# Performance work log

Hardware: AMD Instinct MI355X
Metric: run time of the kernel (lower is better)

The kernel has to match this reference:

```python
import jax, jax.numpy as jnp
import numpy as np

N = 50000      # nodes
E = 800000     # edges (before self-loops)
V = 50000      # vocab
D = 128        # embed_dim
H = 128        # hidden_dim
G = 64         # graphs in batch


def setup_inputs() -> dict:
    key = jax.random.key(0)
    ks = jax.random.split(key, 14)
    x_lex = jax.random.randint(ks[0], (N,), 0, V)
    edge_index = jax.random.randint(ks[1], (2, E), 0, N)
    batch = jnp.sort(jax.random.randint(ks[2], (N,), 0, G))
    s = 1.0 / np.sqrt(D)
    emb = jax.random.normal(ks[3], (V, D), dtype=jnp.float32) * s
    W1 = jax.random.normal(ks[4], (D, H), dtype=jnp.float32) * s
    att_src1 = jax.random.normal(ks[5], (H,), dtype=jnp.float32) * s
    att_dst1 = jax.random.normal(ks[6], (H,), dtype=jnp.float32) * s
    b1 = jnp.zeros((H,), dtype=jnp.float32)
    W2 = jax.random.normal(ks[7], (H, H), dtype=jnp.float32) * s
    att_src2 = jax.random.normal(ks[8], (H,), dtype=jnp.float32) * s
    att_dst2 = jax.random.normal(ks[9], (H,), dtype=jnp.float32) * s
    b2 = jnp.zeros((H,), dtype=jnp.float32)
    Wc = jax.random.normal(ks[10], (H, 1), dtype=jnp.float32) * s
    bc = jnp.zeros((1,), dtype=jnp.float32)
    return dict(x_lex=x_lex, edge_index=edge_index, batch=batch, emb=emb,
                W1=W1, att_src1=att_src1, att_dst1=att_dst1, b1=b1,
                W2=W2, att_src2=att_src2, att_dst2=att_dst2, b2=b2,
                Wc=Wc, bc=bc)


def _gat_conv(x, src, dst, W, a_src, a_dst, b):
    # PyG GATConv, heads=1, self-loops already appended to src/dst.
    h = x @ W                                   # [N, H]
    e = jax.nn.leaky_relu((h @ a_src)[src] + (h @ a_dst)[dst], 0.2)  # [Etot]
    m = jax.ops.segment_max(e, dst, num_segments=N)
    p = jnp.exp(e - m[dst])
    z = jax.ops.segment_sum(p, dst, num_segments=N)
    alpha = p / z[dst]                          # softmax per destination node
    out = jax.ops.segment_sum(alpha[:, None] * h[src], dst, num_segments=N)
    return out + b


def reference(x_lex, edge_index, batch, emb, W1, att_src1, att_dst1, b1,
              W2, att_src2, att_dst2, b2, Wc, bc):
    loops = jnp.arange(N, dtype=edge_index.dtype)
    src = jnp.concatenate([edge_index[0], loops])   # add self-loops (PyG default)
    dst = jnp.concatenate([edge_index[1], loops])
    x = emb[x_lex]                                  # [N, D]
    h = jax.nn.relu(_gat_conv(x, src, dst, W1, att_src1, att_dst1, b1))
    h = jax.nn.relu(_gat_conv(h, src, dst, W2, att_src2, att_dst2, b2))
    sums = jax.ops.segment_sum(h, batch, num_segments=G)           # [G, H]
    cnt = jax.ops.segment_sum(jnp.ones((N,), h.dtype), batch, num_segments=G)
    h_pool = sums / jnp.maximum(cnt, 1.0)[:, None]
    logits = h_pool @ Wc + bc                                       # [G, 1]
    return (logits, h_pool)
```

## Files before the change

kernel.cpp:

```cpp
#include <hip/hip_runtime.h>
#include <hip/hip_bf16.h>


#define THREADS 256
#define PSLICE 16
#define BUK_S 196
#define SORT_BLOCKS 128

typedef __attribute__((ext_vector_type(8))) short short8v;
typedef __attribute__((ext_vector_type(4))) float f32x4;

static __device__ __forceinline__ unsigned short f2bf(float f) {
    unsigned int u = __float_as_uint(f);
    return (unsigned short)((u + 0x7fffu + ((u >> 16) & 1u)) >> 16);
}
static __device__ __forceinline__ float bf2f(unsigned short b) {
    return __uint_as_float(((unsigned int)b) << 16);
}

__global__ __launch_bounds__(THREADS) void k_wsplit2(const float* __restrict__ W1,
                                                     const float* __restrict__ W2,
                                                     unsigned short* __restrict__ Wh1,
                                                     unsigned short* __restrict__ Wl1,
                                                     unsigned short* __restrict__ Wh2,
                                                     unsigned short* __restrict__ Wl2,
                                                     int* __restrict__ bcount, int nbuk) {
    if (blockIdx.x == 0 && threadIdx.x < nbuk) bcount[threadIdx.x] = 0;
    int t = blockIdx.x * THREADS + threadIdx.x;
    const float* W = W1;
    unsigned short* Wh = Wh1;
    unsigned short* Wl = Wl1;
    if (t >= 128 * 128) {
        t -= 128 * 128;
        W = W2; Wh = Wh2; Wl = Wl2;
    }
    int k = t >> 7, n = t & 127;
    float w = W[t];
    unsigned short h = f2bf(w);
    unsigned short lo = f2bf(w - bf2f(h));
    int c = n >> 4, nl = n & 15, tt = k >> 5, kk = k & 31, g = kk >> 3, j = kk & 7;
    int o = (((c * 4 + tt) * 64) + g * 16 + nl) * 8 + j;
    Wh[o] = h;
    Wl[o] = lo;
}

__global__ __launch_bounds__(THREADS) void k_bukhist(const int* __restrict__ dst,
                                                     int* __restrict__ bcount, int E_, int chunk) {
    __shared__ int hist[THREADS];
    hist[threadIdx.x] = 0;
    __syncthreads();
    int e0 = blockIdx.x * chunk;
    int e1 = min(e0 + chunk, E_);
    for (int e = e0 + threadIdx.x; e < e1; e += THREADS)
        atomicAdd(&hist[dst[e] / BUK_S], 1);
    __syncthreads();
    int c = hist[threadIdx.x];
    if (c) atomicAdd(&bcount[threadIdx.x], c);
}

__global__ __launch_bounds__(THREADS) void k_bukscan(const int* __restrict__ bcount,
                                                     int* __restrict__ sbase,
                                                     int* __restrict__ gcur,
                                                     int* __restrict__ cbase,
                                                     int nbuk, int Nn) {
    __shared__ int s[THREADS];
    int tid = threadIdx.x;
    int v = (tid < nbuk) ? bcount[tid] : 0;
    s[tid] = v;
    __syncthreads();
    for (int off = 1; off < THREADS; off <<= 1) {
        int t = (tid >= off) ? s[tid - off] : 0;
        __syncthreads();
        s[tid] += t;
        __syncthreads();
    }
    int excl1 = s[tid] - v;
    if (tid < nbuk) { sbase[tid] = excl1; gcur[tid] = excl1; }
    int n0 = tid * BUK_S;
    int ns = (tid < nbuk) ? min(BUK_S, Nn - n0) : 0;
    int v2 = v + ns;
    __syncthreads();
    s[tid] = v2;
    __syncthreads();
    for (int off = 1; off < THREADS; off <<= 1) {
        int t = (tid >= off) ? s[tid - off] : 0;
        __syncthreads();
        s[tid] += t;
        __syncthreads();
    }
    if (tid < nbuk) cbase[tid] = s[tid] - v2;
}

__global__ __launch_bounds__(THREADS) void k_bukscatter(const int* __restrict__ src,
                                                        const int* __restrict__ dst,
                                                        int* __restrict__ gcur,
                                                        unsigned int* __restrict__ rec,
                                                        int E_, int chunk) {
    __shared__ int hist[THREADS];
    __shared__ int base[THREADS];
    hist[threadIdx.x] = 0;
    __syncthreads();
    int e0 = blockIdx.x * chunk;
    int e1 = min(e0 + chunk, E_);
    for (int e = e0 + threadIdx.x; e < e1; e += THREADS)
        atomicAdd(&hist[dst[e] / BUK_S], 1);
    __syncthreads();
    int c = hist[threadIdx.x];
    if (c) base[threadIdx.x] = atomicAdd(&gcur[threadIdx.x], c);
    hist[threadIdx.x] = 0;
    __syncthreads();
    for (int e = e0 + threadIdx.x; e < e1; e += THREADS) {
        int d = dst[e];
        int b = d / BUK_S;
        int r = atomicAdd(&hist[b], 1);
        rec[base[b] + r] = (unsigned int)src[e] | ((unsigned int)(d - b * BUK_S) << 17);
    }
}

__global__ __launch_bounds__(THREADS) void k_csr(const unsigned int* __restrict__ rec,
                                                 const int* __restrict__ sbase,
                                                 const int* __restrict__ bcount,
                                                 const int* __restrict__ cbase,
                                                 int* __restrict__ rowptr,
                                                 int* __restrict__ esrc,
                                                 int* __restrict__ edst,
                                                 int Nn, int nbuk, int Etot) {
    __shared__ int cnt[THREADS];
    __shared__ int s[THREADS];
    __shared__ int cur[THREADS];
    int b = blockIdx.x;
    int tid = threadIdx.x;
    int n0 = b * BUK_S;
    int ns = min(BUK_S, Nn - n0);
    int cnt_e = bcount[b];
    int rbase = sbase[b];
    int cb = cbase[b];

    cnt[tid] = 0;
    __syncthreads();
    for (int i = tid; i < cnt_e; i += THREADS)
        atomicAdd(&cnt[rec[rbase + i] >> 17], 1);
    __syncthreads();
    int v = (tid < ns) ? cnt[tid] + 1 : 0;
    s[tid] = v;
    __syncthreads();
    for (int off = 1; off < THREADS; off <<= 1) {
        int t = (tid >= off) ? s[tid - off] : 0;
        __syncthreads();
        s[tid] += t;
        __syncthreads();
    }
    int excl = s[tid] - v;
    __syncthreads();
    s[tid] = excl;
    cur[tid] = excl;
    if (tid < ns) rowptr[n0 + tid] = cb + excl;
    if (b == nbuk - 1 && tid == 0) rowptr[Nn] = Etot;
    __syncthreads();
    for (int i = tid; i < cnt_e; i += THREADS) {
        unsigned int r = rec[rbase + i];
        int l = r >> 17;
        int slot = atomicAdd(&cur[l], 1);
        esrc[cb + slot] = (int)(r & 0x1FFFFu);
        edst[cb + slot] = n0 + l;
    }
    __syncthreads();
    if (tid < ns) {
        int slot = s[tid] + cnt[tid];
        esrc[cb + slot] = n0 + tid;
        edst[cb + slot] = n0 + tid;
    }
}

static __device__ __forceinline__ int xsw(int r, int c) {
    return (((r * 16 + (c >> 3)) ^ (r & 7)) << 3) | (c & 7);
}

__global__ __launch_bounds__(THREADS) void k_gemm_mfma(const float* __restrict__ X,
                                                       const int* __restrict__ idx,
                                                       const unsigned short* __restrict__ WBh,
                                                       const unsigned short* __restrict__ WBl,
                                                       const float* __restrict__ a_s,
                                                       const float* __restrict__ a_d,
                                                       unsigned short* __restrict__ outb,
                                                       float* __restrict__ as_,
                                                       float* __restrict__ ad_, int Nrows) {
    __shared__ unsigned short xh[64 * 128];
    __shared__ unsigned short xl[64 * 128];

    {
        int r = threadIdx.x >> 2;
        int c0 = (threadIdx.x & 3) * 32;
        int R = blockIdx.x * 64 + r;
        if (R < Nrows) {
            int g = idx ? idx[R] : R;
            const float4* xrow = (const float4*)(X + (size_t)g * 128);
            #pragma unroll
            for (int i = 0; i < 8; ++i) {
                float4 v = xrow[(c0 >> 2) + i];
                int c = c0 + i * 4;
                ushort4 hh, ll;
                hh.x = f2bf(v.x); ll.x = f2bf(v.x - bf2f(hh.x));
                hh.y = f2bf(v.y); ll.y = f2bf(v.y - bf2f(hh.y));
                hh.z = f2bf(v.z); ll.z = f2bf(v.z - bf2f(hh.z));
                hh.w = f2bf(v.w); ll.w = f2bf(v.w - bf2f(hh.w));
                int o = xsw(r, c);
                *(ushort4*)&xh[o] = hh;
                *(ushort4*)&xl[o] = ll;
            }
        } else {
            #pragma unroll
            for (int i = 0; i < 8; ++i) {
                int o = xsw(r, c0 + i * 4);
                *(ushort4*)&xh[o] = make_ushort4(0, 0, 0, 0);
                *(ushort4*)&xl[o] = make_ushort4(0, 0, 0, 0);
            }
        }
    }
    __syncthreads();

    int wid = threadIdx.x >> 6;
    int lane = threadIdx.x & 63;
    int nl = lane & 15;
    int g = lane >> 4;
    int arow = wid * 16 + nl;

    f32x4 acc[8];
    #pragma unroll
    for (int c = 0; c < 8; ++c) acc[c] = (f32x4){0.f, 0.f, 0.f, 0.f};

    #pragma unroll
    for (int t = 0; t < 4; ++t) {
        int ao = xsw(arow, t * 32 + g * 8);
        short8v ah = *(const short8v*)&xh[ao];
        short8v al = *(const short8v*)&xl[ao];
        #pragma unroll
        for (int c = 0; c < 8; ++c) {
            int bo = (((c * 4 + t) * 64) + lane) * 8;
            short8v bh = *(const short8v*)&WBh[bo];
            short8v bl = *(const short8v*)&WBl[bo];
            acc[c] = __builtin_amdgcn_mfma_f32_16x16x32_bf16(ah, bh, acc[c], 0, 0, 0);
            acc[c] = __builtin_amdgcn_mfma_f32_16x16x32_bf16(ah, bl, acc[c], 0, 0, 0);
            acc[c] = __builtin_amdgcn_mfma_f32_16x16x32_bf16(al, bh, acc[c], 0, 0, 0);
        }
    }

    float asv[8], adv[8];
    #pragma unroll
    for (int c = 0; c < 8; ++c) {
        asv[c] = a_s[c * 16 + nl];
        adv[c] = a_d[c * 16 + nl];
    }
    int Rb = blockIdx.x * 64 + wid * 16 + g * 4;
    #pragma unroll
    for (int r = 0; r < 4; ++r) {
        int R = Rb + r;
        bool ok = (R < Nrows);
        float ps = 0.f, pd = 0.f;
        #pragma unroll
        for (int c = 0; c < 8; ++c) {
            float v = acc[c][r];
            if (ok) outb[(size_t)R * 128 + c * 16 + nl] = f2bf(v);
            ps = fmaf(v, asv[c], ps);
            pd = fmaf(v, adv[c], pd);
        }
        #pragma unroll
        for (int o = 8; o; o >>= 1) {
            ps += __shfl_xor(ps, o);
            pd += __shfl_xor(pd, o);
        }
        if (ok && nl == 0) {
            as_[R] = ps;
            ad_[R] = pd;
        }
    }
}

__global__ __launch_bounds__(THREADS) void k_agg(const unsigned short* __restrict__ hb,
                                                 const float* __restrict__ as_,
                                                 const float* __restrict__ ad_,
                                                 const int* __restrict__ rowptr,
                                                 const int* __restrict__ esrc,
                                                 const float* __restrict__ bias,
                                                 float* __restrict__ out, int Nn) {
    __shared__ int2 ep[4][64];
    int w = threadIdx.x >> 6;
    int lane = threadIdx.x & 63;
    int half = lane >> 5;
    int j = lane & 31;
    int d = blockIdx.x * 4 + w;
    if (d >= Nn) return;
    int beg = rowptr[d], end = rowptr[d + 1];
    float adv = ad_[d];
    float z = 0.f, a0 = 0.f, a1 = 0.f, a2 = 0.f, a3 = 0.f;
    for (int c0 = beg; c0 < end; c0 += 64) {
        int kk = c0 + lane;
        bool ok = (kk < end);
        int sl = esrc[ok ? kk : beg];
        float pv = 0.f;
        if (ok) {
            float e = as_[sl] + adv;
            e = (e > 0.f) ? e : 0.2f * e;
            pv = __expf(e);
        }
        ep[w][lane] = make_int2(sl, __float_as_int(pv));
        int cn = end - c0;
        if (cn > 64) cn = 64;
        for (int k0 = 0; k0 < cn; k0 += 16) {
            int2 ev[8];
            #pragma unroll
            for (int i = 0; i < 8; ++i)
                ev[i] = ep[w][(k0 + 2 * i + half) & 63];
            uint2 hv[8];
            #pragma unroll
            for (int i = 0; i < 8; ++i)
                hv[i] = *(const uint2*)&hb[((size_t)ev[i].x << 7) + j * 4];
            #pragma unroll
            for (int i = 0; i < 8; ++i) {
                float p = __int_as_float(ev[i].y);
                z += p;
                a0 += p * __uint_as_float(hv[i].x << 16);
                a1 += p * __uint_as_float(hv[i].x & 0xffff0000u);
                a2 += p * __uint_as_float(hv[i].y << 16);
                a3 += p * __uint_as_float(hv[i].y & 0xffff0000u);
            }
        }
    }
    z  += __shfl_xor(z, 32);
    a0 += __shfl_xor(a0, 32);
    a1 += __shfl_xor(a1, 32);
    a2 += __shfl_xor(a2, 32);
    a3 += __shfl_xor(a3, 32);
    if (half == 0) {
        float inv = 1.f / z;
        float4 o;
        o.x = fmaxf(a0 * inv + bias[j * 4 + 0], 0.f);
        o.y = fmaxf(a1 * inv + bias[j * 4 + 1], 0.f);
        o.z = fmaxf(a2 * inv + bias[j * 4 + 2], 0.f);
        o.w = fmaxf(a3 * inv + bias[j * 4 + 3], 0.f);
        *(float4*)&out[(size_t)d * 128 + j * 4] = o;
    }
}

__global__ __launch_bounds__(THREADS) void k_pool_partial(const float* __restrict__ x,
                                                          const int* __restrict__ batch,
                                                          float* __restrict__ part, int Nn) {
    int g = blockIdx.x;
    int s = blockIdx.y;
    int a = 0, b = Nn;
    while (a < b) { int mid = (a + b) >> 1; if (batch[mid] < g) a = mid + 1; else b = mid; }
    int lo = a;
    b = Nn;
    while (a < b) { int mid = (a + b) >> 1; if (batch[mid] < g + 1) a = mid + 1; else b = mid; }
    int hi = a;

    int j = threadIdx.x & 127;
    int half = threadIdx.x >> 7;
    float acc = 0.f;
    for (int n = lo + s * 2 + half; n < hi; n += 2 * PSLICE) acc += x[(size_t)n * 128 + j];
    __shared__ float sred[THREADS];
    sred[threadIdx.x] = acc;
    __syncthreads();
    if (half == 0) part[((size_t)g * PSLICE + s) * 128 + j] = sred[j] + sred[128 + j];
}

__global__ __launch_bounds__(128) void k_pool_final(const float* __restrict__ part,
                                                    const int* __restrict__ batch,
                                                    const float* __restrict__ Wc,
                                                    const float* __restrict__ bc,
                                                    float* __restrict__ out, int Nn, int Gn) {
    int g = blockIdx.x;
    int j = threadIdx.x;
    int a = 0, b = Nn;
    while (a < b) { int mid = (a + b) >> 1; if (batch[mid] < g) a = mid + 1; else b = mid; }
    int lo = a;
    b = Nn;
    while (a < b) { int mid = (a + b) >> 1; if (batch[mid] < g + 1) a = mid + 1; else b = mid; }
    int cnt = a - lo;

    float s = 0.f;
    #pragma unroll
    for (int t = 0; t < PSLICE; ++t) s += part[((size_t)g * PSLICE + t) * 128 + j];
    float mean = s / fmaxf((float)cnt, 1.f);
    out[Gn + (size_t)g * 128 + j] = mean;

    __shared__ float sred[128];
    sred[j] = mean * Wc[j];
    __syncthreads();
    for (int off = 64; off >= 1; off >>= 1) {
        if (j < off) sred[j] += sred[j + off];
        __syncthreads();
    }
    if (j == 0) out[g] = sred[0] + bc[0];
}

static inline size_t align256(size_t x) { return (x + 255) & ~(size_t)255; }

extern "C" void kernel_launch(void* const* d_in, const int* in_sizes, int n_in,
                              void* d_out, int out_size, void* d_ws, size_t ws_size,
                              hipStream_t stream) {
    const int* x_lex = (const int*)d_in[0];
    const int* eidx  = (const int*)d_in[1];
    const int* batch = (const int*)d_in[2];
    const float* emb = (const float*)d_in[3];
    const float* W1  = (const float*)d_in[4];
    const float* a_s1 = (const float*)d_in[5];
    const float* a_d1 = (const float*)d_in[6];
    const float* b1  = (const float*)d_in[7];
    const float* W2  = (const float*)d_in[8];
    const float* a_s2 = (const float*)d_in[9];
    const float* a_d2 = (const float*)d_in[10];
    const float* b2  = (const float*)d_in[11];
    const float* Wc  = (const float*)d_in[12];
    const float* bc  = (const float*)d_in[13];

    const int N = in_sizes[0];
    const int E = in_sizes[1] / 2;
    const int G = out_size / 129;
    const int Etot = E + N;
    const int* esrc_in = eidx;
    const int* edst_in = eidx + E;
    const int NBUK = (N + BUK_S - 1) / BUK_S;

    char* p = (char*)d_ws;
    unsigned short* hb = (unsigned short*)p;  p += align256((size_t)N * 128 * 2);
    float* obuf = (float*)p;            p += align256((size_t)N * 128 * 4);
    float* as_  = (float*)p;            p += align256((size_t)N * 4);
    float* ad_  = (float*)p;            p += align256((size_t)N * 4);
    int* bcount = (int*)p;              p += align256((size_t)NBUK * 4);
    int* sbase  = (int*)p;              p += align256((size_t)NBUK * 4);
    int* gcur   = (int*)p;              p += align256((size_t)NBUK * 4);
    int* cbase  = (int*)p;              p += align256((size_t)NBUK * 4);
    int* rowptr = (int*)p;              p += align256((size_t)(N + 1) * 4);
    unsigned int* rec = (unsigned int*)p; p += align256((size_t)Etot * 4);
    int* esrc   = (int*)p;              p += align256((size_t)Etot * 4);
    int* edst   = (int*)p;              p += align256((size_t)Etot * 4);
    float* part = (float*)p;            p += align256((size_t)G * PSLICE * 128 * 4);
    unsigned short* WBh1 = (unsigned short*)p; p += align256((size_t)128 * 128 * 2);
    unsigned short* WBl1 = (unsigned short*)p; p += align256((size_t)128 * 128 * 2);
    unsigned short* WBh2 = (unsigned short*)p; p += align256((size_t)128 * 128 * 2);
    unsigned short* WBl2 = (unsigned short*)p; p += align256((size_t)128 * 128 * 2);

    const int chunk = (E + SORT_BLOCKS - 1) / SORT_BLOCKS;

    k_wsplit2<<<128, THREADS, 0, stream>>>(W1, W2, WBh1, WBl1, WBh2, WBl2, bcount, NBUK);

    k_bukhist<<<SORT_BLOCKS, THREADS, 0, stream>>>(edst_in, bcount, E, chunk);
    k_bukscan<<<1, THREADS, 0, stream>>>(bcount, sbase, gcur, cbase, NBUK, N);
    k_bukscatter<<<SORT_BLOCKS, THREADS, 0, stream>>>(esrc_in, edst_in, gcur, rec, E, chunk);
    k_csr<<<NBUK, THREADS, 0, stream>>>(rec, sbase, bcount, cbase, rowptr, esrc, edst, N, NBUK, Etot);

    const int gemm_grid = (N + 63) / 64;
    const int agg_grid = (N + 3) / 4;

    k_gemm_mfma<<<gemm_grid, THREADS, 0, stream>>>(emb, x_lex, WBh1, WBl1, a_s1, a_d1, hb, as_, ad_, N);
    k_agg<<<agg_grid, THREADS, 0, stream>>>(hb, as_, ad_, rowptr, esrc, b1, obuf, N);

    k_gemm_mfma<<<gemm_grid, THREADS, 0, stream>>>(obuf, nullptr, WBh2, WBl2, a_s2, a_d2, hb, as_, ad_, N);
    k_agg<<<agg_grid, THREADS, 0, stream>>>(hb, as_, ad_, rowptr, esrc, b2, obuf, N);

    k_pool_partial<<<dim3(G, PSLICE), THREADS, 0, stream>>>(obuf, batch, part, N);
    k_pool_final<<<G, 128, 0, stream>>>(part, batch, Wc, bc, (float*)d_out, N, G);
}
```

Measured before the change: 180.5 us.

## Fuse edge histogram and scan into layer-1 GEMM launch, merge pooling kernels

Appends the edge-bucket histogram blocks to the first GEMM grid, so they run alongside it. The last histogram block, detected with an atomic done-counter, performs the bucket scan, which removes the separate histogram and scan launches. The two pooling kernels are merged the same way, with a per-graph last-block finalize, and the unused edst array is no longer written. This cuts three kernel launches and some global writes, in exchange for atomic counters and threadfence ordering, plus counter resets added to the prep kernel.

```diff
diff --git a/kernel.cpp b/kernel.cpp
--- a/kernel.cpp
+++ b/kernel.cpp
@@ -18,14 +18,20 @@
     return __uint_as_float(((unsigned int)b) << 16);
 }
 
-__global__ __launch_bounds__(THREADS) void k_wsplit2(const float* __restrict__ W1,
-                                                     const float* __restrict__ W2,
-                                                     unsigned short* __restrict__ Wh1,
-                                                     unsigned short* __restrict__ Wl1,
-                                                     unsigned short* __restrict__ Wh2,
-                                                     unsigned short* __restrict__ Wl2,
-                                                     int* __restrict__ bcount, int nbuk) {
-    if (blockIdx.x == 0 && threadIdx.x < nbuk) bcount[threadIdx.x] = 0;
+__global__ __launch_bounds__(THREADS) void k_prep(const float* __restrict__ W1,
+                                                  const float* __restrict__ W2,
+                                                  unsigned short* __restrict__ Wh1,
+                                                  unsigned short* __restrict__ Wl1,
+                                                  unsigned short* __restrict__ Wh2,
+                                                  unsigned short* __restrict__ Wl2,
+                                                  int* __restrict__ bcount, int nbuk,
+                                                  int* __restrict__ done,
+                                                  int* __restrict__ pdone, int ng) {
+    if (blockIdx.x == 0) {
+        if (threadIdx.x < nbuk) bcount[threadIdx.x] = 0;
+        if (threadIdx.x == 0) *done = 0;
+        if (threadIdx.x < ng) pdone[threadIdx.x] = 0;
+    }
     int t = blockIdx.x * THREADS + threadIdx.x;
     const float* W = W1;
     unsigned short* Wh = Wh1;
@@ -44,154 +50,25 @@
     Wl[o] = lo;
 }
 
-__global__ __launch_bounds__(THREADS) void k_bukhist(const int* __restrict__ dst,
-                                                     int* __restrict__ bcount, int E_, int chunk) {
-    __shared__ int hist[THREADS];
-    hist[threadIdx.x] = 0;
-    __syncthreads();
-    int e0 = blockIdx.x * chunk;
-    int e1 = min(e0 + chunk, E_);
-    for (int e = e0 + threadIdx.x; e < e1; e += THREADS)
-        atomicAdd(&hist[dst[e] / BUK_S], 1);
-    __syncthreads();
-    int c = hist[threadIdx.x];
-    if (c) atomicAdd(&bcount[threadIdx.x], c);
-}
-
-__global__ __launch_bounds__(THREADS) void k_bukscan(const int* __restrict__ bcount,
-                                                     int* __restrict__ sbase,
-                                                     int* __restrict__ gcur,
-                                                     int* __restrict__ cbase,
-                                                     int nbuk, int Nn) {
-    __shared__ int s[THREADS];
-    int tid = threadIdx.x;
-    int v = (tid < nbuk) ? bcount[tid] : 0;
-    s[tid] = v;
-    __syncthreads();
-    for (int off = 1; off < THREADS; off <<= 1) {
-        int t = (tid >= off) ? s[tid - off] : 0;
-        __syncthreads();
-        s[tid] += t;
-        __syncthreads();
-    }
-    int excl1 = s[tid] - v;
-    if (tid < nbuk) { sbase[tid] = excl1; gcur[tid] = excl1; }
-    int n0 = tid * BUK_S;
-    int ns = (tid < nbuk) ? min(BUK_S, Nn - n0) : 0;
-    int v2 = v + ns;
-    __syncthreads();
-    s[tid] = v2;
-    __syncthreads();
-    for (int off = 1; off < THREADS; off <<= 1) {
-        int t = (tid >= off) ? s[tid - off] : 0;
-        __syncthreads();
-        s[tid] += t;
-        __syncthreads();
-    }
-    if (tid < nbuk) cbase[tid] = s[tid] - v2;
-}
-
-__global__ __launch_bounds__(THREADS) void k_bukscatter(const int* __restrict__ src,
-                                                        const int* __restrict__ dst,
-                                                        int* __restrict__ gcur,
-                                                        unsigned int* __restrict__ rec,
-                                                        int E_, int chunk) {
-    __shared__ int hist[THREADS];
-    __shared__ int base[THREADS];
-    hist[threadIdx.x] = 0;
-    __syncthreads();
-    int e0 = blockIdx.x * chunk;
-    int e1 = min(e0 + chunk, E_);
-    for (int e = e0 + threadIdx.x; e < e1; e += THREADS)
-        atomicAdd(&hist[dst[e] / BUK_S], 1);
-    __syncthreads();
-    int c = hist[threadIdx.x];
-    if (c) base[threadIdx.x] = atomicAdd(&gcur[threadIdx.x], c);
-    hist[threadIdx.x] = 0;
-    __syncthreads();
-    for (int e = e0 + threadIdx.x; e < e1; e += THREADS) {
-        int d = dst[e];
-        int b = d / BUK_S;
-        int r = atomicAdd(&hist[b], 1);
-        rec[base[b] + r] = (unsigned int)src[e] | ((unsigned int)(d - b * BUK_S) << 17);
-    }
-}
-
-__global__ __launch_bounds__(THREADS) void k_csr(const unsigned int* __restrict__ rec,
-                                                 const int* __restrict__ sbase,
-                                                 const int* __restrict__ bcount,
-                                                 const int* __restrict__ cbase,
-                                                 int* __restrict__ rowptr,
-                                                 int* __restrict__ esrc,
-                                                 int* __restrict__ edst,
-                                                 int Nn, int nbuk, int Etot) {
-    __shared__ int cnt[THREADS];
-    __shared__ int s[THREADS];
-    __shared__ int cur[THREADS];
-    int b = blockIdx.x;
-    int tid = threadIdx.x;
-    int n0 = b * BUK_S;
-    int ns = min(BUK_S, Nn - n0);
-    int cnt_e = bcount[b];
-    int rbase = sbase[b];
-    int cb = cbase[b];
-
-    cnt[tid] = 0;
-    __syncthreads();
-    for (int i = tid; i < cnt_e; i += THREADS)
-        atomicAdd(&cnt[rec[rbase + i] >> 17], 1);
-    __syncthreads();
-    int v = (tid < ns) ? cnt[tid] + 1 : 0;
-    s[tid] = v;
-    __syncthreads();
-    for (int off = 1; off < THREADS; off <<= 1) {
-        int t = (tid >= off) ? s[tid - off] : 0;
-        __syncthreads();
-        s[tid] += t;
-        __syncthreads();
-    }
-    int excl = s[tid] - v;
-    __syncthreads();
-    s[tid] = excl;
-    cur[tid] = excl;
-    if (tid < ns) rowptr[n0 + tid] = cb + excl;
-    if (b == nbuk - 1 && tid == 0) rowptr[Nn] = Etot;
-    __syncthreads();
-    for (int i = tid; i < cnt_e; i += THREADS) {
-        unsigned int r = rec[rbase + i];
-        int l = r >> 17;
-        int slot = atomicAdd(&cur[l], 1);
-        esrc[cb + slot] = (int)(r & 0x1FFFFu);
-        edst[cb + slot] = n0 + l;
-    }
-    __syncthreads();
-    if (tid < ns) {
-        int slot = s[tid] + cnt[tid];
-        esrc[cb + slot] = n0 + tid;
-        edst[cb + slot] = n0 + tid;
-    }
-}
-
 static __device__ __forceinline__ int xsw(int r, int c) {
     return (((r * 16 + (c >> 3)) ^ (r & 7)) << 3) | (c & 7);
 }
 
-__global__ __launch_bounds__(THREADS) void k_gemm_mfma(const float* __restrict__ X,
-                                                       const int* __restrict__ idx,
-                                                       const unsigned short* __restrict__ WBh,
-                                                       const unsigned short* __restrict__ WBl,
-                                                       const float* __restrict__ a_s,
-                                                       const float* __restrict__ a_d,
-                                                       unsigned short* __restrict__ outb,
-                                                       float* __restrict__ as_,
-                                                       float* __restrict__ ad_, int Nrows) {
-    __shared__ unsigned short xh[64 * 128];
-    __shared__ unsigned short xl[64 * 128];
-
+static __device__ __forceinline__ void gemm_body(unsigned short* xh, unsigned short* xl,
+                                                 const float* __restrict__ X,
+                                                 const int* __restrict__ idx,
+                                                 const unsigned short* __restrict__ WBh,
+                                                 const unsigned short* __restrict__ WBl,
+                                                 const float* __restrict__ a_s,
+                                                 const float* __restrict__ a_d,
+                                                 unsigned short* __restrict__ outb,
+                                                 float* __restrict__ as_,
+                                                 float* __restrict__ ad_,
+                                                 int Nrows, int bid) {
     {
         int r = threadIdx.x >> 2;
         int c0 = (threadIdx.x & 3) * 32;
-        int R = blockIdx.x * 64 + r;
+        int R = bid * 64 + r;
         if (R < Nrows) {
             int g = idx ? idx[R] : R;
             const float4* xrow = (const float4*)(X + (size_t)g * 128);
@@ -251,7 +128,7 @@
         asv[c] = a_s[c * 16 + nl];
         adv[c] = a_d[c * 16 + nl];
     }
-    int Rb = blockIdx.x * 64 + wid * 16 + g * 4;
+    int Rb = bid * 64 + wid * 16 + g * 4;
     #pragma unroll
     for (int r = 0; r < 4; ++r) {
         int R = Rb + r;
@@ -274,6 +151,165 @@
             ad_[R] = pd;
         }
     }
+}
+
+__global__ __launch_bounds__(THREADS) void k_gemm_hist(const float* __restrict__ X,
+                                                       const int* __restrict__ idx,
+                                                       const unsigned short* __restrict__ WBh,
+                                                       const unsigned short* __restrict__ WBl,
+                                                       const float* __restrict__ a_s,
+                                                       const float* __restrict__ a_d,
+                                                       unsigned short* __restrict__ outb,
+                                                       float* __restrict__ as_,
+                                                       float* __restrict__ ad_,
+                                                       int Nrows, int gemm_blocks,
+                                                       const int* __restrict__ dst,
+                                                       int* __restrict__ bcount,
+                                                       int E_, int chunk,
+                                                       int* __restrict__ done,
+                                                       int* __restrict__ sbase,
+                                                       int* __restrict__ gcur,
+                                                       int* __restrict__ cbase,
+                                                       int nbuk, int Nn) {
+    __shared__ unsigned short xh[64 * 128];
+    __shared__ unsigned short xl[64 * 128];
+    if ((int)blockIdx.x >= gemm_blocks) {
+        int hbk = blockIdx.x - gemm_blocks;
+        int tid = threadIdx.x;
+        __shared__ int hist[THREADS];
+        hist[tid] = 0;
+        __syncthreads();
+        int e0 = hbk * chunk;
+        int e1 = min(e0 + chunk, E_);
+        for (int e = e0 + tid; e < e1; e += THREADS)
+            atomicAdd(&hist[dst[e] / BUK_S], 1);
+        __syncthreads();
+        int c = hist[tid];
+        if (c) atomicAdd(&bcount[tid], c);
+        __threadfence();
+        __syncthreads();
+        __shared__ int lastf;
+        if (tid == 0) lastf = (atomicAdd(done, 1) == SORT_BLOCKS - 1);
+        __syncthreads();
+        if (!lastf) return;
+        __threadfence();
+        __shared__ int s2[THREADS];
+        int v = 0;
+        if (tid < nbuk) v = __hip_atomic_load(&bcount[tid], __ATOMIC_RELAXED, __HIP_MEMORY_SCOPE_AGENT);
+        s2[tid] = v;
+        __syncthreads();
+        for (int off = 1; off < THREADS; off <<= 1) {
+            int t = (tid >= off) ? s2[tid - off] : 0;
+            __syncthreads();
+            s2[tid] += t;
+            __syncthreads();
+        }
+        int excl1 = s2[tid] - v;
+        if (tid < nbuk) { sbase[tid] = excl1; gcur[tid] = excl1; }
+        int n0 = tid * BUK_S;
+        int ns = (tid < nbuk) ? min(BUK_S, Nn - n0) : 0;
+        int v2 = v + ns;
+        __syncthreads();
+        s2[tid] = v2;
+        __syncthreads();
+        for (int off = 1; off < THREADS; off <<= 1) {
+            int t = (tid >= off) ? s2[tid - off] : 0;
+            __syncthreads();
+            s2[tid] += t;
+            __syncthreads();
+        }
+        if (tid < nbuk) cbase[tid] = s2[tid] - v2;
+        return;
+    }
+    gemm_body(xh, xl, X, idx, WBh, WBl, a_s, a_d, outb, as_, ad_, Nrows, blockIdx.x);
+}
+
+__global__ __launch_bounds__(THREADS) void k_gemm_mfma(const float* __restrict__ X,
+                                                       const unsigned short* __restrict__ WBh,
+                                                       const unsigned short* __restrict__ WBl,
+                                                       const float* __restrict__ a_s,
+                                                       const float* __restrict__ a_d,
+                                                       unsigned short* __restrict__ outb,
+                                                       float* __restrict__ as_,
+                                                       float* __restrict__ ad_, int Nrows) {
+    __shared__ unsigned short xh[64 * 128];
+    __shared__ unsigned short xl[64 * 128];
+    gemm_body(xh, xl, X, nullptr, WBh, WBl, a_s, a_d, outb, as_, ad_, Nrows, blockIdx.x);
+}
+
+__global__ __launch_bounds__(THREADS) void k_bukscatter(const int* __restrict__ src,
+                                                        const int* __restrict__ dst,
+                                                        int* __restrict__ gcur,
+                                                        unsigned int* __restrict__ rec,
+                                                        int E_, int chunk) {
+    __shared__ int hist[THREADS];
+    __shared__ int base[THREADS];
+    hist[threadIdx.x] = 0;
+    __syncthreads();
+    int e0 = blockIdx.x * chunk;
+    int e1 = min(e0 + chunk, E_);
+    for (int e = e0 + threadIdx.x; e < e1; e += THREADS)
+        atomicAdd(&hist[dst[e] / BUK_S], 1);
+    __syncthreads();
+    int c = hist[threadIdx.x];
+    if (c) base[threadIdx.x] = atomicAdd(&gcur[threadIdx.x], c);
+    hist[threadIdx.x] = 0;
+    __syncthreads();
+    for (int e = e0 + threadIdx.x; e < e1; e += THREADS) {
+        int d = dst[e];
+        int b = d / BUK_S;
+        int r = atomicAdd(&hist[b], 1);
+        rec[base[b] + r] = (unsigned int)src[e] | ((unsigned int)(d - b * BUK_S) << 17);
+    }
+}
+
+__global__ __launch_bounds__(THREADS) void k_csr(const unsigned int* __restrict__ rec,
+                                                 const int* __restrict__ sbase,
+                                                 const int* __restrict__ bcount,
+                                                 const int* __restrict__ cbase,
+                                                 int* __restrict__ rowptr,
+                                                 int* __restrict__ esrc,
+                                                 int Nn, int nbuk, int Etot) {
+    __shared__ int cnt[THREADS];
+    __shared__ int s[THREADS];
+    __shared__ int cur[THREADS];
+    int b = blockIdx.x;
+    int tid = threadIdx.x;
+    int n0 = b * BUK_S;
+    int ns = min(BUK_S, Nn - n0);
+    int cnt_e = bcount[b];
+    int rbase = sbase[b];
+    int cb = cbase[b];
+
+    cnt[tid] = 0;
+    __syncthreads();
+    for (int i = tid; i < cnt_e; i += THREADS)
+        atomicAdd(&cnt[rec[rbase + i] >> 17], 1);
+    __syncthreads();
+    int v = (tid < ns) ? cnt[tid] + 1 : 0;
+    s[tid] = v;
+    __syncthreads();
+    for (int off = 1; off < THREADS; off <<= 1) {
+        int t = (tid >= off) ? s[tid - off] : 0;
+        __syncthreads();
+        s[tid] += t;
+        __syncthreads();
+    }
+    int excl = s[tid] - v;
+    __syncthreads();
+    s[tid] = excl;
+    cur[tid] = excl;
+    if (tid < ns) rowptr[n0 + tid] = cb + excl;
+    if (b == nbuk - 1 && tid == 0) rowptr[Nn] = Etot;
+    __syncthreads();
+    for (int i = tid; i < cnt_e; i += THREADS) {
+        unsigned int r = rec[rbase + i];
+        int l = r >> 17;
+        int slot = atomicAdd(&cur[l], 1);
+        esrc[cb + slot] = (int)(r & 0x1FFFFu);
+    }
+    __syncthreads();
+    if (tid < ns) esrc[cb + s[tid] + cnt[tid]] = n0 + tid;
 }
 
 __global__ __launch_bounds__(THREADS) void k_agg(const unsigned short* __restrict__ hb,
@@ -342,9 +378,13 @@
     }
 }
 
-__global__ __launch_bounds__(THREADS) void k_pool_partial(const float* __restrict__ x,
-                                                          const int* __restrict__ batch,
-                                                          float* __restrict__ part, int Nn) {
+__global__ __launch_bounds__(THREADS) void k_pool(const float* __restrict__ x,
+                                                  const int* __restrict__ batch,
+                                                  float* __restrict__ part,
+                                                  int* __restrict__ pdone,
+                                                  const float* __restrict__ Wc,
+                                                  const float* __restrict__ bc,
+                                                  float* __restrict__ out, int Nn, int Gn) {
     int g = blockIdx.x;
     int s = blockIdx.y;
     int a = 0, b = Nn;
@@ -354,44 +394,40 @@
     while (a < b) { int mid = (a + b) >> 1; if (batch[mid] < g + 1) a = mid + 1; else b = mid; }
     int hi = a;
 
+    __shared__ float sred[THREADS];
     int j = threadIdx.x & 127;
     int half = threadIdx.x >> 7;
     float acc = 0.f;
     for (int n = lo + s * 2 + half; n < hi; n += 2 * PSLICE) acc += x[(size_t)n * 128 + j];
-    __shared__ float sred[THREADS];
     sred[threadIdx.x] = acc;
     __syncthreads();
     if (half == 0) part[((size_t)g * PSLICE + s) * 128 + j] = sred[j] + sred[128 + j];
-}
-
-__global__ __launch_bounds__(128) void k_pool_final(const float* __restrict__ part,
-                                                    const int* __restrict__ batch,
-                                                    const float* __restrict__ Wc,
-                                                    const float* __restrict__ bc,
-                                                    float* __restrict__ out, int Nn, int Gn) {
-    int g = blockIdx.x;
-    int j = threadIdx.x;
-    int a = 0, b = Nn;
-    while (a < b) { int mid = (a + b) >> 1; if (batch[mid] < g) a = mid + 1; else b = mid; }
-    int lo = a;
-    b = Nn;
-    while (a < b) { int mid = (a + b) >> 1; if (batch[mid] < g + 1) a = mid + 1; else b = mid; }
-    int cnt = a - lo;
-
-    float s = 0.f;
-    #pragma unroll
-    for (int t = 0; t < PSLICE; ++t) s += part[((size_t)g * PSLICE + t) * 128 + j];
-    float mean = s / fmaxf((float)cnt, 1.f);
-    out[Gn + (size_t)g * 128 + j] = mean;
-
-    __shared__ float sred[128];
-    sred[j] = mean * Wc[j];
+    __threadfence();
+    __syncthreads();
+    __shared__ int lastf;
+    if (threadIdx.x == 0) lastf = (atomicAdd(&pdone[g], 1) == PSLICE - 1);
+    __syncthreads();
+    if (!lastf) return;
+    __threadfence();
+    int cnt = hi - lo;
+    float mean = 0.f;
+    if (half == 0) {
+        float ssum = 0.f;
+        #pragma unroll
+        for (int t = 0; t < PSLICE; ++t)
+            ssum += __hip_atomic_load(&part[((size_t)g * PSLICE + t) * 128 + j],
+                                      __ATOMIC_RELAXED, __HIP_MEMORY_SCOPE_AGENT);
+        mean = ssum / fmaxf((float)cnt, 1.f);
+        out[Gn + (size_t)g * 128 + j] = mean;
+    }
+    __syncthreads();
+    if (half == 0) sred[j] = mean * Wc[j];
     __syncthreads();
     for (int off = 64; off >= 1; off >>= 1) {
-        if (j < off) sred[j] += sred[j + off];
-        __syncthreads();
-    }
-    if (j == 0) out[g] = sred[0] + bc[0];
+        if (threadIdx.x < off) sred[threadIdx.x] += sred[threadIdx.x + off];
+        __syncthreads();
+    }
+    if (threadIdx.x == 0) out[g] = sred[0] + bc[0];
 }
 
 static inline size_t align256(size_t x) { return (x + 255) & ~(size_t)255; }
@@ -431,10 +467,11 @@
     int* sbase  = (int*)p;              p += align256((size_t)NBUK * 4);
     int* gcur   = (int*)p;              p += align256((size_t)NBUK * 4);
     int* cbase  = (int*)p;              p += align256((size_t)NBUK * 4);
+    int* done   = (int*)p;              p += align256(256);
+    int* pdone  = (int*)p;              p += align256((size_t)G * 4);
     int* rowptr = (int*)p;              p += align256((size_t)(N + 1) * 4);
     unsigned int* rec = (unsigned int*)p; p += align256((size_t)Etot * 4);
     int* esrc   = (int*)p;              p += align256((size_t)Etot * 4);
-    int* edst   = (int*)p;              p += align256((size_t)Etot * 4);
     float* part = (float*)p;            p += align256((size_t)G * PSLICE * 128 * 4);
     unsigned short* WBh1 = (unsigned short*)p; p += align256((size_t)128 * 128 * 2);
     unsigned short* WBl1 = (unsigned short*)p; p += align256((size_t)128 * 128 * 2);
@@ -442,23 +479,22 @@
     unsigned short* WBl2 = (unsigned short*)p; p += align256((size_t)128 * 128 * 2);
 
     const int chunk = (E + SORT_BLOCKS - 1) / SORT_BLOCKS;
-
-    k_wsplit2<<<128, THREADS, 0, stream>>>(W1, W2, WBh1, WBl1, WBh2, WBl2, bcount, NBUK);
-
-    k_bukhist<<<SORT_BLOCKS, THREADS, 0, stream>>>(edst_in, bcount, E, chunk);
-    k_bukscan<<<1, THREADS, 0, stream>>>(bcount, sbase, gcur, cbase, NBUK, N);
-    k_bukscatter<<<SORT_BLOCKS, THREADS, 0, stream>>>(esrc_in, edst_in, gcur, rec, E, chunk);
-    k_csr<<<NBUK, THREADS, 0, stream>>>(rec, sbase, bcount, cbase, rowptr, esrc, edst, N, NBUK, Etot);
-
     const int gemm_grid = (N + 63) / 64;
     const int agg_grid = (N + 3) / 4;
 
-    k_gemm_mfma<<<gemm_grid, THREADS, 0, stream>>>(emb, x_lex, WBh1, WBl1, a_s1, a_d1, hb, as_, ad_, N);
+    k_prep<<<128, THREADS, 0, stream>>>(W1, W2, WBh1, WBl1, WBh2, WBl2, bcount, NBUK, done, pdone, G);
+
+    k_gemm_hist<<<gemm_grid + SORT_BLOCKS, THREADS, 0, stream>>>(
+        emb, x_lex, WBh1, WBl1, a_s1, a_d1, hb, as_, ad_, N, gemm_grid,
+        edst_in, bcount, E, chunk, done, sbase, gcur, cbase, NBUK, N);
+
+    k_bukscatter<<<SORT_BLOCKS, THREADS, 0, stream>>>(esrc_in, edst_in, gcur, rec, E, chunk);
+    k_csr<<<NBUK, THREADS, 0, stream>>>(rec, sbase, bcount, cbase, rowptr, esrc, N, NBUK, Etot);
+
     k_agg<<<agg_grid, THREADS, 0, stream>>>(hb, as_, ad_, rowptr, esrc, b1, obuf, N);
 
-    k_gemm_mfma<<<gemm_grid, THREADS, 0, stream>>>(obuf, nullptr, WBh2, WBl2, a_s2, a_d2, hb, as_, ad_, N);
+    k_gemm_mfma<<<gemm_grid, THREADS, 0, stream>>>(obuf, WBh2, WBl2, a_s2, a_d2, hb, as_, ad_, N);
     k_agg<<<agg_grid, THREADS, 0, stream>>>(hb, as_, ad_, rowptr, esrc, b2, obuf, N);
 
-    k_pool_partial<<<dim3(G, PSLICE), THREADS, 0, stream>>>(obuf, batch, part, N);
-    k_pool_final<<<G, 128, 0, stream>>>(part, batch, Wc, bc, (float*)d_out, N, G);
-}
+    k_pool<<<dim3(G, PSLICE), THREADS, 0, stream>>>(obuf, batch, part, pdone, Wc, bc, (float*)d_out, N, G);
+}
```

Measured after the change: 253.9 us. +40.7%, slower.
